# Optimization experiments

Hardware: AMD Instinct MI355X
Metric: run time of the kernel (lower is better)

The kernel has to match this reference:

```python
import jax, jax.numpy as jnp
import numpy as np

N_NODES, N_EDGES, EMB_DIM = 100000, 1000000, 64
NUM_BOND_TYPE, NUM_BOND_DIR = 6, 3  # self-loop bond type index = 4


def gcn_conv(x, src, dst, bond_type, bond_dir, W, b, emb_bond, emb_dir):
    """One GCNConv (Hu et al. mol-GNN variant). src/dst/attrs already include self-loops."""
    N = x.shape[0]
    edge_emb = emb_bond[bond_type] + emb_dir[bond_dir]           # [Etot, D]
    ones = jnp.ones(src.shape[0], x.dtype)
    deg = jax.ops.segment_sum(ones, src, num_segments=N)         # scatter_add over row
    dis = jnp.where(deg > 0, jax.lax.rsqrt(deg), 0.0)
    norm = dis[src] * dis[dst]                                   # [Etot]
    h = x @ W.T + b                                              # [N, D]
    msg = norm[:, None] * (h[src] + edge_emb)                    # [Etot, D]
    return jax.ops.segment_sum(msg, dst, num_segments=N)         # add-aggregate at target


def with_self_loops(edge_index, edge_attr, N):
    loop = jnp.arange(N, dtype=edge_index.dtype)
    src = jnp.concatenate([edge_index[0], loop])
    dst = jnp.concatenate([edge_index[1], loop])
    bt = jnp.concatenate([edge_attr[:, 0], jnp.full((N,), 4, edge_attr.dtype)])
    bd = jnp.concatenate([edge_attr[:, 1], jnp.zeros((N,), edge_attr.dtype)])
    return src, dst, bt, bd


def setup_inputs() -> dict:
    key = jax.random.key(0)
    ks = jax.random.split(key, 12)
    D = EMB_DIM
    s = 1.0 / np.sqrt(D)
    inp = {
        "x": jax.random.normal(ks[0], (N_NODES, D), jnp.float32),
        "edge_index": jax.random.randint(ks[1], (2, N_EDGES), 0, N_NODES, jnp.int64 if jax.config.jax_enable_x64 else jnp.int32),
        "edge_attr": jax.random.randint(ks[2], (N_EDGES, 2), 0, 3, jnp.int64 if jax.config.jax_enable_x64 else jnp.int32),
        "W1": jax.random.uniform(ks[3], (D, D), jnp.float32, -s, s),
        "b1": jax.random.uniform(ks[4], (D,), jnp.float32, -s, s),
        "ebond1": jax.random.normal(ks[5], (NUM_BOND_TYPE, D), jnp.float32) * 0.1,
        "edir1": jax.random.normal(ks[6], (NUM_BOND_DIR, D), jnp.float32) * 0.1,
        "W2": jax.random.uniform(ks[7], (D, D), jnp.float32, -s, s),
        "b2": jax.random.uniform(ks[8], (D,), jnp.float32, -s, s),
        "ebond2": jax.random.normal(ks[9], (NUM_BOND_TYPE, D), jnp.float32) * 0.1,
        "edir2": jax.random.normal(ks[10], (NUM_BOND_DIR, D), jnp.float32) * 0.1,
    }
    return inp


def reference(x, edge_index, edge_attr, W1, b1, ebond1, edir1, W2, b2, ebond2, edir2):
    N = x.shape[0]
    src, dst, bt, bd = with_self_loops(edge_index, edge_attr, N)
    h = gcn_conv(x, src, dst, bt, bd, W1, b1, ebond1, edir1)
    h = jax.nn.relu(h)
    out = gcn_conv(h, src, dst, bt, bd, W2, b2, ebond2, edir2)
    return out
```

## Files before the change

kernel.cpp:

```cpp
#include <hip/hip_runtime.h>


#define THREADS 256
#define MAXNBC 512
#define BCAP 4096
#define CHUNK 2048
#define GEMM_SMEM_BYTES (64 * 68 * 4)

typedef __attribute__((ext_vector_type(8))) short bf16x8;
typedef __attribute__((ext_vector_type(4))) float f32x4;

__device__ __forceinline__ float bflo(unsigned int v) { return __uint_as_float(v << 16); }
__device__ __forceinline__ float bfhi(unsigned int v) { return __uint_as_float(v & 0xFFFF0000u); }
__device__ __forceinline__ unsigned short f2bf(float f) {
    unsigned int u = __float_as_uint(f);
    return (unsigned short)((u + 0x7FFFu + ((u >> 16) & 1u)) >> 16);
}
__device__ __forceinline__ int sb(unsigned int w, int j) {
    return (int)(w << (24 - 8 * j)) >> 24;
}

template <bool XBF16>
__device__ __forceinline__ void gemm64_body(int tile, const void* __restrict__ Xv,
                                            const float* __restrict__ W,
                                            const float* __restrict__ B,
                                            unsigned short* __restrict__ Hb,
                                            unsigned char* __restrict__ Hq,
                                            float2* __restrict__ dsc, int N,
                                            float (*smem)[68]) {
    int t = threadIdx.x;
    int lane = t & 63;
    int wave = __builtin_amdgcn_readfirstlane(t >> 6);
    int l15 = lane & 15;
    int lk = lane >> 4;
    int arow = tile * 64 + wave * 16 + l15;

    bf16x8 a0, a1;
    if (arow < N) {
        if (XBF16) {
            const unsigned short* xp = (const unsigned short*)Xv + (size_t)arow * 64 + 8 * lk;
            a0 = *(const bf16x8*)xp;
            a1 = *(const bf16x8*)(xp + 32);
        } else {
            const float* xp = (const float*)Xv + (size_t)arow * 64 + 8 * lk;
            float4 v0 = *(const float4*)xp;
            float4 v1 = *(const float4*)(xp + 4);
            float4 v2 = *(const float4*)(xp + 32);
            float4 v3 = *(const float4*)(xp + 36);
            a0[0] = (short)f2bf(v0.x); a0[1] = (short)f2bf(v0.y);
            a0[2] = (short)f2bf(v0.z); a0[3] = (short)f2bf(v0.w);
            a0[4] = (short)f2bf(v1.x); a0[5] = (short)f2bf(v1.y);
            a0[6] = (short)f2bf(v1.z); a0[7] = (short)f2bf(v1.w);
            a1[0] = (short)f2bf(v2.x); a1[1] = (short)f2bf(v2.y);
            a1[2] = (short)f2bf(v2.z); a1[3] = (short)f2bf(v2.w);
            a1[4] = (short)f2bf(v3.x); a1[5] = (short)f2bf(v3.y);
            a1[6] = (short)f2bf(v3.z); a1[7] = (short)f2bf(v3.w);
        }
    } else {
#pragma unroll
        for (int e = 0; e < 8; ++e) { a0[e] = 0; a1[e] = 0; }
    }

    bf16x8 bfr[4][2];
#pragma unroll
    for (int n = 0; n < 4; ++n) {
        const float* wp = W + (size_t)(16 * n + l15) * 64 + 8 * lk;
#pragma unroll
        for (int ks = 0; ks < 2; ++ks) {
            float4 u0 = *(const float4*)(wp + 32 * ks);
            float4 u1 = *(const float4*)(wp + 32 * ks + 4);
            bf16x8 bb;
            bb[0] = (short)f2bf(u0.x); bb[1] = (short)f2bf(u0.y);
            bb[2] = (short)f2bf(u0.z); bb[3] = (short)f2bf(u0.w);
            bb[4] = (short)f2bf(u1.x); bb[5] = (short)f2bf(u1.y);
            bb[6] = (short)f2bf(u1.z); bb[7] = (short)f2bf(u1.w);
            bfr[n][ks] = bb;
        }
    }

    f32x4 acc[4];
#pragma unroll
    for (int n = 0; n < 4; ++n) {
        f32x4 z = {0.0f, 0.0f, 0.0f, 0.0f};
        z = __builtin_amdgcn_mfma_f32_16x16x32_bf16(a0, bfr[n][0], z, 0, 0, 0);
        acc[n] = __builtin_amdgcn_mfma_f32_16x16x32_bf16(a1, bfr[n][1], z, 0, 0, 0);
    }

#pragma unroll
    for (int n = 0; n < 4; ++n) {
        float bv = B[16 * n + l15];
        int col = 16 * n + l15;
#pragma unroll
        for (int r = 0; r < 4; ++r)
            smem[16 * wave + 4 * lk + r][col] = acc[n][r] + bv;
    }
    __syncthreads();

#pragma unroll
    for (int i = 0; i < 2; ++i) {
        int idx = t + i * THREADS;
        int r = idx >> 3;
        int c8 = (idx & 7) << 3;
        int grow = tile * 64 + r;
        float4 va = *(const float4*)(&smem[r][c8]);
        float4 vb = *(const float4*)(&smem[r][c8 + 4]);
        float v[8] = {va.x, va.y, va.z, va.w, vb.x, vb.y, vb.z, vb.w};
        float m = fabsf(v[0]);
#pragma unroll
        for (int j = 1; j < 8; ++j) m = fmaxf(m, fabsf(v[j]));
        m = fmaxf(m, __shfl_xor(m, 1));
        m = fmaxf(m, __shfl_xor(m, 2));
        m = fmaxf(m, __shfl_xor(m, 4));
        if (grow < N) {
            uint4 o;
            o.x = (unsigned)f2bf(v[0]) | ((unsigned)f2bf(v[1]) << 16);
            o.y = (unsigned)f2bf(v[2]) | ((unsigned)f2bf(v[3]) << 16);
            o.z = (unsigned)f2bf(v[4]) | ((unsigned)f2bf(v[5]) << 16);
            o.w = (unsigned)f2bf(v[6]) | ((unsigned)f2bf(v[7]) << 16);
            *(uint4*)(Hb + (size_t)grow * 64 + c8) = o;
            float inv = m > 0.0f ? 127.0f / m : 0.0f;
            int q[8];
#pragma unroll
            for (int j = 0; j < 8; ++j) q[j] = __float2int_rn(v[j] * inv);
            uint2 qp;
            qp.x = (unsigned)(q[0] & 255) | ((unsigned)(q[1] & 255) << 8) |
                   ((unsigned)(q[2] & 255) << 16) | ((unsigned)(q[3] & 255) << 24);
            qp.y = (unsigned)(q[4] & 255) | ((unsigned)(q[5] & 255) << 8) |
                   ((unsigned)(q[6] & 255) << 16) | ((unsigned)(q[7] & 255) << 24);
            *(uint2*)(Hq + (size_t)grow * 64 + c8) = qp;
            if ((idx & 7) == 0) dsc[grow].y = m * (1.0f / 127.0f);
        }
    }
}

__global__ __launch_bounds__(THREADS) void zero_gemm_kernel(
    int* __restrict__ gcur, int ncur, const float* __restrict__ X,
    const float* __restrict__ W1, const float* __restrict__ B1,
    unsigned short* __restrict__ Hb, unsigned char* __restrict__ Hq,
    float2* __restrict__ dsc, int N, int tile0) {
    __shared__ __align__(16) char sh[GEMM_SMEM_BYTES];
    int b = blockIdx.x;
    if (b == 0) {
        for (int i = threadIdx.x; i < ncur; i += THREADS) gcur[i] = 0;
        return;
    }
    gemm64_body<false>(tile0 + b - 1, X, W1, B1, Hb, Hq, dsc, N, (float(*)[68])sh);
}

__global__ __launch_bounds__(THREADS) void scatter_kernel(
    const int* __restrict__ src, const int* __restrict__ dst, const int* __restrict__ attr,
    int* __restrict__ gcurS, int* __restrict__ gcurD, unsigned char* __restrict__ payS,
    unsigned int* __restrict__ payD, int E, int NBC, int SCB,
    const float* __restrict__ X, const float* __restrict__ W1, const float* __restrict__ B1,
    unsigned short* __restrict__ Hb, unsigned char* __restrict__ Hq,
    float2* __restrict__ dsc, int N, int tile0) {
    __shared__ __align__(16) char sh[GEMM_SMEM_BYTES];
    int b = blockIdx.x;
    if (b >= SCB) {
        gemm64_body<false>(tile0 + b - SCB, X, W1, B1, Hb, Hq, dsc, N, (float(*)[68])sh);
        return;
    }
    int* hS = (int*)sh;
    int* hD = hS + MAXNBC;
    int t = threadIdx.x;
    for (int k = t; k < NBC; k += THREADS) {
        hS[k] = 0;
        hD[k] = 0;
    }
    __syncthreads();
    int lo = b * CHUNK, hi = min(E, lo + CHUNK);
    for (int i = lo + t; i < hi; i += THREADS) {
        atomicAdd(&hS[src[i] >> 8], 1);
        atomicAdd(&hD[dst[i] >> 8], 1);
    }
    __syncthreads();
    for (int k = t; k < NBC; k += THREADS) {
        int h = hS[k];
        int base = h ? atomicAdd(&gcurS[k], h) : 0;
        hS[k] = k * BCAP + base;
        int hd = hD[k];
        int bd = hd ? atomicAdd(&gcurD[k], hd) : 0;
        hD[k] = k * BCAP + bd;
    }
    __syncthreads();
    const int2* ap = (const int2*)attr;
    for (int i = lo + t; i < hi; i += THREADS) {
        int sv = src[i], dv = dst[i];
        int2 a = ap[i];
        int pS = atomicAdd(&hS[sv >> 8], 1);
        payS[pS] = (unsigned char)(sv & 255);
        int pD = atomicAdd(&hD[dv >> 8], 1);
        payD[pD] = (unsigned int)sv | ((unsigned int)(a.x * 3 + a.y) << 17) |
                   ((unsigned int)(dv & 255) << 22);
    }
}

__global__ __launch_bounds__(THREADS) void build_kernel(
    const unsigned char* __restrict__ payS, const unsigned int* __restrict__ payD,
    const int* __restrict__ gcurS, const int* __restrict__ gcurD,
    unsigned int* __restrict__ sorted, int* __restrict__ row_ptr, int* __restrict__ cnt_out,
    int NBC, const float* __restrict__ X, const float* __restrict__ W1,
    const float* __restrict__ B1, unsigned short* __restrict__ Hb,
    unsigned char* __restrict__ Hq, float2* __restrict__ dsc, int N, int tile0) {
    __shared__ __align__(16) char sh[GEMM_SMEM_BYTES];
    int b = blockIdx.x;
    if (b >= 2 * NBC) {
        gemm64_body<false>(tile0 + b - 2 * NBC, X, W1, B1, Hb, Hq, dsc, N, (float(*)[68])sh);
        return;
    }
    int t = threadIdx.x;
    if (b < NBC) {
        int k = b;
        int* cnt = (int*)sh;
        cnt[t] = 0;
        __syncthreads();
        int n = gcurS[k], off = k * BCAP;
        for (int i = t; i < n; i += THREADS) atomicAdd(&cnt[payS[off + i]], 1);
        __syncthreads();
        int node = k * 256 + t;
        if (node < N) dsc[node].x = 1.0f / sqrtf(1.0f + (float)cnt[t]);
    } else {
        int k = b - NBC;
        int* cnt = (int*)sh;
        int* cur = cnt + 256;
        int* s = cur + 256;
        cnt[t] = 0;
        __syncthreads();
        int ecnt = gcurD[k], eoff = k * BCAP;
        for (int i = t; i < ecnt; i += THREADS)
            atomicAdd(&cnt[(payD[eoff + i] >> 22) & 255], 1);
        __syncthreads();
        int v = cnt[t];
        s[t] = v;
        __syncthreads();
        for (int d = 1; d < THREADS; d <<= 1) {
            int a = (t >= d) ? s[t - d] : 0;
            __syncthreads();
            s[t] += a;
            __syncthreads();
        }
        int excl = s[t] - v;
        int node = k * 256 + t;
        if (node < N) {
            row_ptr[node] = eoff + excl;
            cnt_out[node] = v;
        }
        cur[t] = excl;
        __syncthreads();
        for (int i = t; i < ecnt; i += THREADS) {
            unsigned int u = payD[eoff + i];
            int p = atomicAdd(&cur[(u >> 22) & 255], 1);
            sorted[eoff + p] = u & 0x3FFFFFu;
        }
    }
}

template <bool XBF16>
__global__ __launch_bounds__(THREADS) void gemm64_kernel(const void* __restrict__ Xv,
                                                         const float* __restrict__ W,
                                                         const float* __restrict__ B,
                                                         unsigned short* __restrict__ Hb,
                                                         unsigned char* __restrict__ Hq,
                                                         float2* __restrict__ dsc, int N) {
    __shared__ __align__(16) char sh[GEMM_SMEM_BYTES];
    gemm64_body<XBF16>(blockIdx.x, Xv, W, B, Hb, Hq, dsc, N, (float(*)[68])sh);
}

__device__ __forceinline__ void edge_acc(unsigned int u, float dn,
                                         const float2* __restrict__ dsc,
                                         const unsigned char* __restrict__ Hq, int c,
                                         const float (*embc)[64], float acc[8]) {
    int s0 = u & 0x1FFFF;
    int e0 = (u >> 17) & 31;
    float2 ds = dsc[s0];
    uint2 q = *(const uint2*)(Hq + (size_t)s0 * 64 + c);
    float w = ds.x * dn, ws = w * ds.y;
    float4 ea = *(const float4*)(&embc[e0][c]);
    float4 eb = *(const float4*)(&embc[e0][c + 4]);
    acc[0] = fmaf(ws, (float)sb(q.x, 0), fmaf(w, ea.x, acc[0]));
    acc[1] = fmaf(ws, (float)sb(q.x, 1), fmaf(w, ea.y, acc[1]));
    acc[2] = fmaf(ws, (float)sb(q.x, 2), fmaf(w, ea.z, acc[2]));
    acc[3] = fmaf(ws, (float)sb(q.x, 3), fmaf(w, ea.w, acc[3]));
    acc[4] = fmaf(ws, (float)sb(q.y, 0), fmaf(w, eb.x, acc[4]));
    acc[5] = fmaf(ws, (float)sb(q.y, 1), fmaf(w, eb.y, acc[5]));
    acc[6] = fmaf(ws, (float)sb(q.y, 2), fmaf(w, eb.z, acc[6]));
    acc[7] = fmaf(ws, (float)sb(q.y, 3), fmaf(w, eb.w, acc[7]));
}

template <bool RELU_BF16_OUT>
__global__ __launch_bounds__(THREADS) void aggregate_kernel(
    const unsigned short* __restrict__ Hb, const unsigned char* __restrict__ Hq,
    const float2* __restrict__ dsc, const float* __restrict__ ebond,
    const float* __restrict__ edir, const int* __restrict__ row_ptr,
    const int* __restrict__ cnt, const unsigned int* __restrict__ entries,
    void* __restrict__ outv, int N) {
    __shared__ float embc[18][64];
    int t = threadIdx.x;
    for (int i = t; i < 18 * 64; i += THREADS) {
        int row = i >> 6, c = i & 63;
        embc[row][c] = ebond[(row / 3) * 64 + c] + edir[(row % 3) * 64 + c];
    }
    __syncthreads();

    int n = blockIdx.x * 32 + (t >> 3);
    if (n >= N) return;
    int c = (t & 7) << 3;

    float dn = dsc[n].x;
    uint4 hv = *(const uint4*)(Hb + (size_t)n * 64 + c);
    float4 ea = *(const float4*)(&embc[12][c]);
    float4 eb = *(const float4*)(&embc[12][c + 4]);
    float nrm = dn * dn;
    float accA[8], accB[8];
    accA[0] = nrm * (bflo(hv.x) + ea.x);
    accA[1] = nrm * (bfhi(hv.x) + ea.y);
    accA[2] = nrm * (bflo(hv.y) + ea.z);
    accA[3] = nrm * (bfhi(hv.y) + ea.w);
    accA[4] = nrm * (bflo(hv.z) + eb.x);
    accA[5] = nrm * (bfhi(hv.z) + eb.y);
    accA[6] = nrm * (bflo(hv.w) + eb.z);
    accA[7] = nrm * (bfhi(hv.w) + eb.w);
#pragma unroll
    for (int j = 0; j < 8; ++j) accB[j] = 0.0f;

    int p = row_ptr[n];
    int end = p + cnt[n];
    const float(*ec)[64] = (const float(*)[64])embc;
    for (; p + 3 < end; p += 4) {
        unsigned int u0 = entries[p];
        unsigned int u1 = entries[p + 1];
        unsigned int u2 = entries[p + 2];
        unsigned int u3 = entries[p + 3];
        edge_acc(u0, dn, dsc, Hq, c, ec, accA);
        edge_acc(u1, dn, dsc, Hq, c, ec, accB);
        edge_acc(u2, dn, dsc, Hq, c, ec, accA);
        edge_acc(u3, dn, dsc, Hq, c, ec, accB);
    }
    for (; p < end; ++p) edge_acc(entries[p], dn, dsc, Hq, c, ec, accA);

    float o[8];
#pragma unroll
    for (int j = 0; j < 8; ++j) o[j] = accA[j] + accB[j];

    if (RELU_BF16_OUT) {
        unsigned short* ob = (unsigned short*)outv;
        uint4 ov;
        ov.x = (unsigned)f2bf(fmaxf(o[0], 0.0f)) | ((unsigned)f2bf(fmaxf(o[1], 0.0f)) << 16);
        ov.y = (unsigned)f2bf(fmaxf(o[2], 0.0f)) | ((unsigned)f2bf(fmaxf(o[3], 0.0f)) << 16);
        ov.z = (unsigned)f2bf(fmaxf(o[4], 0.0f)) | ((unsigned)f2bf(fmaxf(o[5], 0.0f)) << 16);
        ov.w = (unsigned)f2bf(fmaxf(o[6], 0.0f)) | ((unsigned)f2bf(fmaxf(o[7], 0.0f)) << 16);
        *(uint4*)(ob + (size_t)n * 64 + c) = ov;
    } else {
        float* of = (float*)outv;
        *(float4*)(of + (size_t)n * 64 + c) = make_float4(o[0], o[1], o[2], o[3]);
        *(float4*)(of + (size_t)n * 64 + c + 4) = make_float4(o[4], o[5], o[6], o[7]);
    }
}

extern "C" void kernel_launch(void* const* d_in, const int* in_sizes, int n_in,
                              void* d_out, int out_size, void* d_ws, size_t ws_size,
                              hipStream_t stream) {
    const float* x      = (const float*)d_in[0];
    const int*   eidx   = (const int*)d_in[1];
    const int*   eattr  = (const int*)d_in[2];
    const float* W1     = (const float*)d_in[3];
    const float* b1     = (const float*)d_in[4];
    const float* ebond1 = (const float*)d_in[5];
    const float* edir1  = (const float*)d_in[6];
    const float* W2     = (const float*)d_in[7];
    const float* b2     = (const float*)d_in[8];
    const float* ebond2 = (const float*)d_in[9];
    const float* edir2  = (const float*)d_in[10];

    const int N = in_sizes[0] / 64;
    const int E = in_sizes[1] / 2;
    const int* src = eidx;
    const int* dst = eidx + E;
    float* out = (float*)d_out;
    const int NBC = (N + 255) >> 8;
    const int SCB = (E + CHUNK - 1) / CHUNK;

    char* w = (char*)d_ws;
    size_t Na = ((size_t)N * 4 + 255) & ~(size_t)255;
    float2* dsc    = (float2*)w;           w += 2 * Na;
    int*   row_ptr = (int*)w;              w += Na;
    int*   cnt     = (int*)w;              w += Na;
    int*   gcur    = (int*)w;              w += 2 * MAXNBC * 4;
    unsigned int* payD   = (unsigned int*)w;   w += (size_t)MAXNBC * BCAP * 4;
    unsigned int* sorted = (unsigned int*)w;   w += (size_t)MAXNBC * BCAP * 4;
    unsigned char* payS  = (unsigned char*)w;  w += (size_t)MAXNBC * BCAP;
    unsigned short* Hb   = (unsigned short*)w; w += (size_t)N * 64 * 2;
    unsigned char*  Hq   = (unsigned char*)w;  w += ((size_t)N * 64 + 255) & ~(size_t)255;
    unsigned short* Ab   = (unsigned short*)w; w += (size_t)N * 64 * 2;
    int* gcurS = gcur;
    int* gcurD = gcur + MAXNBC;

    const int gT   = (N + 63) / 64;
    const int gN32 = (N + 31) / 32;

    const int t0 = min(gT, 256);
    const int t1 = min(gT - t0, 512);
    const int t2 = gT - t0 - t1;

    zero_gemm_kernel<<<1 + t0, THREADS, 0, stream>>>(gcur, 2 * MAXNBC, x, W1, b1, Hb, Hq,
                                                     dsc, N, 0);
    scatter_kernel<<<SCB + t1, THREADS, 0, stream>>>(src, dst, eattr, gcurS, gcurD, payS,
                                                     payD, E, NBC, SCB, x, W1, b1, Hb, Hq,
                                                     dsc, N, t0);
    build_kernel<<<2 * NBC + t2, THREADS, 0, stream>>>(payS, payD, gcurS, gcurD, sorted,
                                                       row_ptr, cnt, NBC, x, W1, b1, Hb, Hq,
                                                       dsc, N, t0 + t1);

    aggregate_kernel<true><<<gN32, THREADS, 0, stream>>>(Hb, Hq, dsc, ebond1, edir1, row_ptr,
                                                         cnt, sorted, Ab, N);

    gemm64_kernel<true><<<gT, THREADS, 0, stream>>>(Ab, W2, b2, Hb, Hq, dsc, N);
    aggregate_kernel<false><<<gN32, THREADS, 0, stream>>>(Hb, Hq, dsc, ebond2, edir2, row_ptr,
                                                          cnt, sorted, out, N);
}
```

Baseline: 228.8 us.

## Locally sort edge chunks in shared memory before coalesced bucket scatter

After: 230.9 us. No clear change (+1.0%).

```diff
diff --git a/kernel.cpp b/kernel.cpp
--- a/kernel.cpp
+++ b/kernel.cpp
@@ -2,10 +2,12 @@
 
 
 #define THREADS 256
-#define MAXNBC 512
-#define BCAP 4096
-#define CHUNK 2048
+#define MAXNB 128
+#define BCAP 16384
+#define SCAP 4096
+#define CHUNK 4096
 #define GEMM_SMEM_BYTES (64 * 68 * 4)
+#define SC_SMEM (4 * CHUNK * 2 + CHUNK * 2 + 9 * 128 * 4)
 
 typedef __attribute__((ext_vector_type(8))) short bf16x8;
 typedef __attribute__((ext_vector_type(4))) float f32x4;
@@ -149,86 +151,153 @@
 
 __global__ __launch_bounds__(THREADS) void scatter_kernel(
     const int* __restrict__ src, const int* __restrict__ dst, const int* __restrict__ attr,
-    int* __restrict__ gcurS, int* __restrict__ gcurD, unsigned char* __restrict__ payS,
-    unsigned int* __restrict__ payD, int E, int NBC, int SCB,
+    int* __restrict__ gcurS, int* __restrict__ gcurD, unsigned short* __restrict__ payS,
+    unsigned int* __restrict__ payD, int E, int SCB,
     const float* __restrict__ X, const float* __restrict__ W1, const float* __restrict__ B1,
     unsigned short* __restrict__ Hb, unsigned char* __restrict__ Hq,
     float2* __restrict__ dsc, int N, int tile0) {
-    __shared__ __align__(16) char sh[GEMM_SMEM_BYTES];
+    __shared__ __align__(16) char sh[SC_SMEM];
     int b = blockIdx.x;
     if (b >= SCB) {
         gemm64_body<false>(tile0 + b - SCB, X, W1, B1, Hb, Hq, dsc, N, (float(*)[68])sh);
         return;
     }
-    int* hS = (int*)sh;
-    int* hD = hS + MAXNBC;
+    unsigned int* Wv  = (unsigned int*)sh;
+    unsigned int* SD  = Wv + CHUNK;
+    unsigned char* DB = (unsigned char*)(SD + CHUNK);
+    unsigned char* SDB = DB + CHUNK;
+    int* hD   = (int*)(SDB + CHUNK);
+    int* hS   = hD + 128;
+    int* loD  = hS + 128;
+    int* loS  = loD + 128;
+    int* mapD = loS + 128;
+    int* mapS = mapD + 128;
+    int* curD = mapS + 128;
+    int* curS = curD + 128;
+    int* scn  = curS + 128;
+    unsigned short* SS = (unsigned short*)Wv;
+    unsigned char* SSB = DB;
+
     int t = threadIdx.x;
-    for (int k = t; k < NBC; k += THREADS) {
-        hS[k] = 0;
-        hD[k] = 0;
-    }
-    __syncthreads();
+    if (t < 128) { hD[t] = 0; hS[t] = 0; }
+    __syncthreads();
+
     int lo = b * CHUNK, hi = min(E, lo + CHUNK);
-    for (int i = lo + t; i < hi; i += THREADS) {
-        atomicAdd(&hS[src[i] >> 8], 1);
-        atomicAdd(&hD[dst[i] >> 8], 1);
-    }
-    __syncthreads();
-    for (int k = t; k < NBC; k += THREADS) {
-        int h = hS[k];
-        int base = h ? atomicAdd(&gcurS[k], h) : 0;
-        hS[k] = k * BCAP + base;
-        int hd = hD[k];
-        int bd = hd ? atomicAdd(&gcurD[k], hd) : 0;
-        hD[k] = k * BCAP + bd;
-    }
-    __syncthreads();
+    int nch = hi - lo;
     const int2* ap = (const int2*)attr;
-    for (int i = lo + t; i < hi; i += THREADS) {
+    for (int li = t; li < nch; li += THREADS) {
+        int i = lo + li;
         int sv = src[i], dv = dst[i];
         int2 a = ap[i];
-        int pS = atomicAdd(&hS[sv >> 8], 1);
-        payS[pS] = (unsigned char)(sv & 255);
-        int pD = atomicAdd(&hD[dv >> 8], 1);
-        payD[pD] = (unsigned int)sv | ((unsigned int)(a.x * 3 + a.y) << 17) |
-                   ((unsigned int)(dv & 255) << 22);
+        Wv[li] = (unsigned int)sv | ((unsigned int)(a.x * 3 + a.y) << 17) |
+                 ((unsigned int)(dv & 1023) << 22);
+        DB[li] = (unsigned char)(dv >> 10);
+        atomicAdd(&hD[dv >> 10], 1);
+        atomicAdd(&hS[sv >> 10], 1);
+    }
+    __syncthreads();
+
+    if (t < 128) {
+        int h = hD[t];
+        int r = h ? atomicAdd(&gcurD[t], h) : 0;
+        mapD[t] = t * BCAP + r;
+        int h2 = hS[t];
+        int r2 = h2 ? atomicAdd(&gcurS[t], h2) : 0;
+        mapS[t] = t * BCAP + r2;
+    }
+    if (t < 128) scn[t] = hD[t];
+    __syncthreads();
+    for (int d = 1; d < 128; d <<= 1) {
+        int a = (t >= d && t < 128) ? scn[t - d] : 0;
+        __syncthreads();
+        if (t < 128) scn[t] += a;
+        __syncthreads();
+    }
+    if (t < 128) {
+        int e = scn[t] - hD[t];
+        loD[t] = e;
+        curD[t] = e;
+        mapD[t] -= e;
+        scn[t] = hS[t];
+    }
+    __syncthreads();
+    for (int d = 1; d < 128; d <<= 1) {
+        int a = (t >= d && t < 128) ? scn[t - d] : 0;
+        __syncthreads();
+        if (t < 128) scn[t] += a;
+        __syncthreads();
+    }
+    if (t < 128) {
+        int e = scn[t] - hS[t];
+        loS[t] = e;
+        curS[t] = e;
+        mapS[t] -= e;
+    }
+    __syncthreads();
+
+    for (int li = t; li < nch; li += THREADS) {
+        int k = DB[li];
+        int p = atomicAdd(&curD[k], 1);
+        SD[p] = Wv[li];
+        SDB[p] = (unsigned char)k;
+    }
+    __syncthreads();
+
+    for (int li = t; li < nch; li += THREADS) {
+        int val = (int)(SD[li] & 0x1FFFFu);
+        int k = val >> 10;
+        int p = atomicAdd(&curS[k], 1);
+        SS[p] = (unsigned short)(val & 1023);
+        SSB[p] = (unsigned char)k;
+    }
+    __syncthreads();
+
+    for (int li = t; li < nch; li += THREADS) {
+        payD[mapD[SDB[li]] + li] = SD[li];
+        payS[mapS[SSB[li]] + li] = SS[li];
     }
 }
 
 __global__ __launch_bounds__(THREADS) void build_kernel(
-    const unsigned char* __restrict__ payS, const unsigned int* __restrict__ payD,
+    const unsigned short* __restrict__ payS, const unsigned int* __restrict__ payD,
     const int* __restrict__ gcurS, const int* __restrict__ gcurD,
     unsigned int* __restrict__ sorted, int* __restrict__ row_ptr, int* __restrict__ cnt_out,
-    int NBC, const float* __restrict__ X, const float* __restrict__ W1,
+    int NB, const float* __restrict__ X, const float* __restrict__ W1,
     const float* __restrict__ B1, unsigned short* __restrict__ Hb,
     unsigned char* __restrict__ Hq, float2* __restrict__ dsc, int N, int tile0) {
     __shared__ __align__(16) char sh[GEMM_SMEM_BYTES];
     int b = blockIdx.x;
-    if (b >= 2 * NBC) {
-        gemm64_body<false>(tile0 + b - 2 * NBC, X, W1, B1, Hb, Hq, dsc, N, (float(*)[68])sh);
+    if (b >= 8 * NB) {
+        gemm64_body<false>(tile0 + b - 8 * NB, X, W1, B1, Hb, Hq, dsc, N, (float(*)[68])sh);
         return;
     }
     int t = threadIdx.x;
-    if (b < NBC) {
-        int k = b;
+    if (b < 4 * NB) {
+        int k = b >> 2, j = b & 3;
         int* cnt = (int*)sh;
         cnt[t] = 0;
         __syncthreads();
         int n = gcurS[k], off = k * BCAP;
-        for (int i = t; i < n; i += THREADS) atomicAdd(&cnt[payS[off + i]], 1);
-        __syncthreads();
-        int node = k * 256 + t;
+        for (int i = t; i < n; i += THREADS) {
+            int val = payS[off + i];
+            if ((val >> 8) == j) atomicAdd(&cnt[val & 255], 1);
+        }
+        __syncthreads();
+        int node = k * 1024 + j * 256 + t;
         if (node < N) dsc[node].x = 1.0f / sqrtf(1.0f + (float)cnt[t]);
     } else {
-        int k = b - NBC;
+        int b2 = b - 4 * NB;
+        int k = b2 >> 2, j = b2 & 3;
         int* cnt = (int*)sh;
         int* cur = cnt + 256;
         int* s = cur + 256;
         cnt[t] = 0;
         __syncthreads();
         int ecnt = gcurD[k], eoff = k * BCAP;
-        for (int i = t; i < ecnt; i += THREADS)
-            atomicAdd(&cnt[(payD[eoff + i] >> 22) & 255], 1);
+        for (int i = t; i < ecnt; i += THREADS) {
+            unsigned int d10 = payD[eoff + i] >> 22;
+            if ((int)(d10 >> 8) == j) atomicAdd(&cnt[d10 & 255], 1);
+        }
         __syncthreads();
         int v = cnt[t];
         s[t] = v;
@@ -240,17 +309,21 @@
             __syncthreads();
         }
         int excl = s[t] - v;
-        int node = k * 256 + t;
+        int obase = (4 * k + j) * SCAP;
+        int node = k * 1024 + j * 256 + t;
         if (node < N) {
-            row_ptr[node] = eoff + excl;
+            row_ptr[node] = obase + excl;
             cnt_out[node] = v;
         }
         cur[t] = excl;
         __syncthreads();
         for (int i = t; i < ecnt; i += THREADS) {
             unsigned int u = payD[eoff + i];
-            int p = atomicAdd(&cur[(u >> 22) & 255], 1);
-            sorted[eoff + p] = u & 0x3FFFFFu;
+            unsigned int d10 = u >> 22;
+            if ((int)(d10 >> 8) == j) {
+                int p = atomicAdd(&cur[d10 & 255], 1);
+                sorted[obase + p] = u & 0x3FFFFFu;
+            }
         }
     }
 }
@@ -377,7 +450,7 @@
     const int* src = eidx;
     const int* dst = eidx + E;
     float* out = (float*)d_out;
-    const int NBC = (N + 255) >> 8;
+    const int NB = (N + 1023) >> 10;
     const int SCB = (E + CHUNK - 1) / CHUNK;
 
     char* w = (char*)d_ws;
@@ -385,15 +458,15 @@
     float2* dsc    = (float2*)w;           w += 2 * Na;
     int*   row_ptr = (int*)w;              w += Na;
     int*   cnt     = (int*)w;              w += Na;
-    int*   gcur    = (int*)w;              w += 2 * MAXNBC * 4;
-    unsigned int* payD   = (unsigned int*)w;   w += (size_t)MAXNBC * BCAP * 4;
-    unsigned int* sorted = (unsigned int*)w;   w += (size_t)MAXNBC * BCAP * 4;
-    unsigned char* payS  = (unsigned char*)w;  w += (size_t)MAXNBC * BCAP;
+    int*   gcur    = (int*)w;              w += 2 * MAXNB * 4;
+    unsigned int* payD   = (unsigned int*)w;   w += (size_t)MAXNB * BCAP * 4;
+    unsigned int* sorted = (unsigned int*)w;   w += (size_t)4 * MAXNB * SCAP * 4;
+    unsigned short* payS = (unsigned short*)w; w += (size_t)MAXNB * BCAP * 2;
     unsigned short* Hb   = (unsigned short*)w; w += (size_t)N * 64 * 2;
     unsigned char*  Hq   = (unsigned char*)w;  w += ((size_t)N * 64 + 255) & ~(size_t)255;
     unsigned short* Ab   = (unsigned short*)w; w += (size_t)N * 64 * 2;
     int* gcurS = gcur;
-    int* gcurD = gcur + MAXNBC;
+    int* gcurD = gcur + MAXNB;
 
     const int gT   = (N + 63) / 64;
     const int gN32 = (N + 31) / 32;
@@ -402,14 +475,14 @@
     const int t1 = min(gT - t0, 512);
     const int t2 = gT - t0 - t1;
 
-    zero_gemm_kernel<<<1 + t0, THREADS, 0, stream>>>(gcur, 2 * MAXNBC, x, W1, b1, Hb, Hq,
+    zero_gemm_kernel<<<1 + t0, THREADS, 0, stream>>>(gcur, 2 * MAXNB, x, W1, b1, Hb, Hq,
                                                      dsc, N, 0);
     scatter_kernel<<<SCB + t1, THREADS, 0, stream>>>(src, dst, eattr, gcurS, gcurD, payS,
-                                                     payD, E, NBC, SCB, x, W1, b1, Hb, Hq,
+                                                     payD, E, SCB, x, W1, b1, Hb, Hq,
                                                      dsc, N, t0);
-    build_kernel<<<2 * NBC + t2, THREADS, 0, stream>>>(payS, payD, gcurS, gcurD, sorted,
-                                                       row_ptr, cnt, NBC, x, W1, b1, Hb, Hq,
-                                                       dsc, N, t0 + t1);
+    build_kernel<<<8 * NB + t2, THREADS, 0, stream>>>(payS, payD, gcurS, gcurD, sorted,
+                                                      row_ptr, cnt, NB, x, W1, b1, Hb, Hq,
+                                                      dsc, N, t0 + t1);
 
     aggregate_kernel<true><<<gN32, THREADS, 0, stream>>>(Hb, Hq, dsc, ebond1, edir1, row_ptr,
                                                          cnt, sorted, Ab, N);
```

## Locally sort scatter chunks in shared memory for coalesced bucket writes

Applied to the files above, without the earlier changes.

Result: faster. 221.6 us (-3.1%).

```diff
diff --git a/kernel.cpp b/kernel.cpp
--- a/kernel.cpp
+++ b/kernel.cpp
@@ -2,10 +2,11 @@
 
 
 #define THREADS 256
-#define MAXNBC 512
+#define NBINS 512
 #define BCAP 4096
 #define CHUNK 2048
 #define GEMM_SMEM_BYTES (64 * 68 * 4)
+#define SC_SMEM (CHUNK * 4 * 2 + CHUNK * 2 * 2 + 6 * NBINS * 4 + 256 * 4)
 
 typedef __attribute__((ext_vector_type(8))) short bf16x8;
 typedef __attribute__((ext_vector_type(4))) float f32x4;
@@ -150,48 +151,112 @@
 __global__ __launch_bounds__(THREADS) void scatter_kernel(
     const int* __restrict__ src, const int* __restrict__ dst, const int* __restrict__ attr,
     int* __restrict__ gcurS, int* __restrict__ gcurD, unsigned char* __restrict__ payS,
-    unsigned int* __restrict__ payD, int E, int NBC, int SCB,
+    unsigned int* __restrict__ payD, int E, int SCB,
     const float* __restrict__ X, const float* __restrict__ W1, const float* __restrict__ B1,
     unsigned short* __restrict__ Hb, unsigned char* __restrict__ Hq,
     float2* __restrict__ dsc, int N, int tile0) {
-    __shared__ __align__(16) char sh[GEMM_SMEM_BYTES];
+    __shared__ __align__(16) char sh[SC_SMEM];
     int b = blockIdx.x;
     if (b >= SCB) {
         gemm64_body<false>(tile0 + b - SCB, X, W1, B1, Hb, Hq, dsc, N, (float(*)[68])sh);
         return;
     }
-    int* hS = (int*)sh;
-    int* hD = hS + MAXNBC;
+    unsigned int* Wv = (unsigned int*)sh;
+    unsigned int* SD = Wv + CHUNK;
+    unsigned short* DB = (unsigned short*)(SD + CHUNK);
+    unsigned short* SDB = DB + CHUNK;
+    int* hD = (int*)(SDB + CHUNK);
+    int* hS = hD + NBINS;
+    int* mapD = hS + NBINS;
+    int* mapS = mapD + NBINS;
+    int* curD = mapS + NBINS;
+    int* curS = curD + NBINS;
+    int* scn = curS + NBINS;
+    unsigned char* SS = (unsigned char*)Wv;
+    unsigned short* SSB = DB;
+
     int t = threadIdx.x;
-    for (int k = t; k < NBC; k += THREADS) {
-        hS[k] = 0;
-        hD[k] = 0;
-    }
-    __syncthreads();
+    for (int k = t; k < NBINS; k += THREADS) { hD[k] = 0; hS[k] = 0; }
+    __syncthreads();
+
     int lo = b * CHUNK, hi = min(E, lo + CHUNK);
-    for (int i = lo + t; i < hi; i += THREADS) {
-        atomicAdd(&hS[src[i] >> 8], 1);
-        atomicAdd(&hD[dst[i] >> 8], 1);
-    }
-    __syncthreads();
-    for (int k = t; k < NBC; k += THREADS) {
-        int h = hS[k];
-        int base = h ? atomicAdd(&gcurS[k], h) : 0;
-        hS[k] = k * BCAP + base;
-        int hd = hD[k];
-        int bd = hd ? atomicAdd(&gcurD[k], hd) : 0;
-        hD[k] = k * BCAP + bd;
-    }
-    __syncthreads();
+    int nch = hi - lo;
     const int2* ap = (const int2*)attr;
-    for (int i = lo + t; i < hi; i += THREADS) {
+    for (int li = t; li < nch; li += THREADS) {
+        int i = lo + li;
         int sv = src[i], dv = dst[i];
         int2 a = ap[i];
-        int pS = atomicAdd(&hS[sv >> 8], 1);
-        payS[pS] = (unsigned char)(sv & 255);
-        int pD = atomicAdd(&hD[dv >> 8], 1);
-        payD[pD] = (unsigned int)sv | ((unsigned int)(a.x * 3 + a.y) << 17) |
-                   ((unsigned int)(dv & 255) << 22);
+        Wv[li] = (unsigned int)sv | ((unsigned int)(a.x * 3 + a.y) << 17) |
+                 ((unsigned int)(dv & 255) << 22);
+        DB[li] = (unsigned short)(dv >> 8);
+        atomicAdd(&hD[dv >> 8], 1);
+        atomicAdd(&hS[sv >> 8], 1);
+    }
+    __syncthreads();
+
+    for (int k = t; k < NBINS; k += THREADS) {
+        int h = hD[k];
+        int r = h ? atomicAdd(&gcurD[k], h) : 0;
+        mapD[k] = k * BCAP + r;
+        int h2 = hS[k];
+        int r2 = h2 ? atomicAdd(&gcurS[k], h2) : 0;
+        mapS[k] = k * BCAP + r2;
+    }
+    __syncthreads();
+
+    scn[t] = hD[2 * t] + hD[2 * t + 1];
+    __syncthreads();
+    for (int d = 1; d < THREADS; d <<= 1) {
+        int a = (t >= d) ? scn[t - d] : 0;
+        __syncthreads();
+        scn[t] += a;
+        __syncthreads();
+    }
+    {
+        int off = t ? scn[t - 1] : 0;
+        curD[2 * t] = off;
+        curD[2 * t + 1] = off + hD[2 * t];
+        mapD[2 * t] -= off;
+        mapD[2 * t + 1] -= off + hD[2 * t];
+    }
+    __syncthreads();
+    scn[t] = hS[2 * t] + hS[2 * t + 1];
+    __syncthreads();
+    for (int d = 1; d < THREADS; d <<= 1) {
+        int a = (t >= d) ? scn[t - d] : 0;
+        __syncthreads();
+        scn[t] += a;
+        __syncthreads();
+    }
+    {
+        int off = t ? scn[t - 1] : 0;
+        curS[2 * t] = off;
+        curS[2 * t + 1] = off + hS[2 * t];
+        mapS[2 * t] -= off;
+        mapS[2 * t + 1] -= off + hS[2 * t];
+    }
+    __syncthreads();
+
+    for (int li = t; li < nch; li += THREADS) {
+        int k = DB[li];
+        int p = atomicAdd(&curD[k], 1);
+        SD[p] = Wv[li];
+        SDB[p] = (unsigned short)k;
+    }
+    __syncthreads();
+
+    for (int li = t; li < nch; li += THREADS) {
+        int val = (int)(SD[li] & 0x1FFFFu);
+        int k = val >> 8;
+        int p = atomicAdd(&curS[k], 1);
+        SS[p] = (unsigned char)(val & 255);
+        SSB[p] = (unsigned short)k;
+    }
+    __syncthreads();
+
+    for (int li = t; li < nch; li += THREADS) {
+        payD[mapD[SDB[li]] + li] = SD[li];
+        payS[mapS[SSB[li]] + li] = SS[li];
     }
 }
 
@@ -199,19 +264,14 @@
     const unsigned char* __restrict__ payS, const unsigned int* __restrict__ payD,
     const int* __restrict__ gcurS, const int* __restrict__ gcurD,
     unsigned int* __restrict__ sorted, int* __restrict__ row_ptr, int* __restrict__ cnt_out,
-    int NBC, const float* __restrict__ X, const float* __restrict__ W1,
-    const float* __restrict__ B1, unsigned short* __restrict__ Hb,
-    unsigned char* __restrict__ Hq, float2* __restrict__ dsc, int N, int tile0) {
-    __shared__ __align__(16) char sh[GEMM_SMEM_BYTES];
+    int NB2, float2* __restrict__ dsc, int N) {
+    __shared__ int cnt[256];
+    __shared__ int cur[256];
+    __shared__ int s[THREADS];
+    int t = threadIdx.x;
     int b = blockIdx.x;
-    if (b >= 2 * NBC) {
-        gemm64_body<false>(tile0 + b - 2 * NBC, X, W1, B1, Hb, Hq, dsc, N, (float(*)[68])sh);
-        return;
-    }
-    int t = threadIdx.x;
-    if (b < NBC) {
+    if (b < NB2) {
         int k = b;
-        int* cnt = (int*)sh;
         cnt[t] = 0;
         __syncthreads();
         int n = gcurS[k], off = k * BCAP;
@@ -220,10 +280,7 @@
         int node = k * 256 + t;
         if (node < N) dsc[node].x = 1.0f / sqrtf(1.0f + (float)cnt[t]);
     } else {
-        int k = b - NBC;
-        int* cnt = (int*)sh;
-        int* cur = cnt + 256;
-        int* s = cur + 256;
+        int k = b - NB2;
         cnt[t] = 0;
         __syncthreads();
         int ecnt = gcurD[k], eoff = k * BCAP;
@@ -377,7 +434,7 @@
     const int* src = eidx;
     const int* dst = eidx + E;
     float* out = (float*)d_out;
-    const int NBC = (N + 255) >> 8;
+    const int NB2 = (N + 255) >> 8;
     const int SCB = (E + CHUNK - 1) / CHUNK;
 
     char* w = (char*)d_ws;
@@ -385,31 +442,29 @@
     float2* dsc    = (float2*)w;           w += 2 * Na;
     int*   row_ptr = (int*)w;              w += Na;
     int*   cnt     = (int*)w;              w += Na;
-    int*   gcur    = (int*)w;              w += 2 * MAXNBC * 4;
-    unsigned int* payD   = (unsigned int*)w;   w += (size_t)MAXNBC * BCAP * 4;
-    unsigned int* sorted = (unsigned int*)w;   w += (size_t)MAXNBC * BCAP * 4;
-    unsigned char* payS  = (unsigned char*)w;  w += (size_t)MAXNBC * BCAP;
+    int*   gcur    = (int*)w;              w += 2 * NBINS * 4;
+    unsigned int* payD   = (unsigned int*)w;   w += (size_t)NBINS * BCAP * 4;
+    unsigned int* sorted = (unsigned int*)w;   w += (size_t)NBINS * BCAP * 4;
+    unsigned char* payS  = (unsigned char*)w;  w += (size_t)NBINS * BCAP;
     unsigned short* Hb   = (unsigned short*)w; w += (size_t)N * 64 * 2;
     unsigned char*  Hq   = (unsigned char*)w;  w += ((size_t)N * 64 + 255) & ~(size_t)255;
     unsigned short* Ab   = (unsigned short*)w; w += (size_t)N * 64 * 2;
     int* gcurS = gcur;
-    int* gcurD = gcur + MAXNBC;
+    int* gcurD = gcur + NBINS;
 
     const int gT   = (N + 63) / 64;
     const int gN32 = (N + 31) / 32;
 
-    const int t0 = min(gT, 256);
-    const int t1 = min(gT - t0, 512);
-    const int t2 = gT - t0 - t1;
-
-    zero_gemm_kernel<<<1 + t0, THREADS, 0, stream>>>(gcur, 2 * MAXNBC, x, W1, b1, Hb, Hq,
+    const int t0 = min(gT, 512);
+    const int t1 = gT - t0;
+
+    zero_gemm_kernel<<<1 + t0, THREADS, 0, stream>>>(gcur, 2 * NBINS, x, W1, b1, Hb, Hq,
                                                      dsc, N, 0);
     scatter_kernel<<<SCB + t1, THREADS, 0, stream>>>(src, dst, eattr, gcurS, gcurD, payS,
-                                                     payD, E, NBC, SCB, x, W1, b1, Hb, Hq,
+                                                     payD, E, SCB, x, W1, b1, Hb, Hq,
                                                      dsc, N, t0);
-    build_kernel<<<2 * NBC + t2, THREADS, 0, stream>>>(payS, payD, gcurS, gcurD, sorted,
-                                                       row_ptr, cnt, NBC, x, W1, b1, Hb, Hq,
-                                                       dsc, N, t0 + t1);
+    build_kernel<<<2 * NB2, THREADS, 0, stream>>>(payS, payD, gcurS, gcurD, sorted,
+                                                  row_ptr, cnt, NB2, dsc, N);
 
     aggregate_kernel<true><<<gN32, THREADS, 0, stream>>>(Hb, Hq, dsc, ebond1, edir1, row_ptr,
                                                          cnt, sorted, Ab, N);
```
